# Kernel optimization log

Hardware: AMD Instinct MI355X
Metric: run time of the kernel (lower is better)

## Reference

```python
import jax, jax.numpy as jnp
import numpy as np

EPS = 1e-5

def inorm(x):
    # instance norm over time (last) axis; torch.std is unbiased (ddof=1)
    m = jnp.mean(x, axis=-1, keepdims=True)
    s = jnp.sqrt(jnp.var(x, axis=-1, ddof=1, keepdims=True))
    return (x - m) / (s + EPS)

def tinorm(x):
    # time-wise instance norm: normalize over channel axis (dim=1)
    m = jnp.mean(x, axis=1, keepdims=True)
    s = jnp.sqrt(jnp.var(x, axis=1, ddof=1, keepdims=True))
    return (x - m) / (s + EPS)

def adaptive_norm(src, trg, wq, wk, wv, norm_fn):
    # src, trg: [B,C,T]; wq/wk/wv: [out,in] as in nn.Linear
    temp = src.shape[1] ** 0.5
    q = jnp.einsum('bct,oc->bto', norm_fn(src), wq)        # [B,Ts,C]
    k = jnp.einsum('bct,oc->bto', norm_fn(trg), wk)        # [B,Tt,C]
    v = jnp.einsum('bct,oc->bto', trg, wv)                 # [B,Tt,C]
    attn = jax.nn.softmax(jnp.einsum('bsc,btc->bst', q / temp, k), axis=-1)
    mean = jnp.einsum('bst,btc->bsc', attn, v)             # attn-weighted mean
    var = jax.nn.relu(jnp.einsum('bst,btc->bsc', attn, v * v) - mean * mean)
    mean_c = jnp.mean(mean, axis=1)[:, :, None]            # [B,C,1]
    std_c = jnp.sqrt(jnp.mean(var, axis=1))[:, :, None]    # [B,C,1]
    return std_c * inorm(src) + mean_c

def sap(x, w, b):
    # self-attention pooling over axis 1; x: [B,N,C], w: [C], b: [1]
    a = jax.nn.softmax(jnp.einsum('bnc,c->bn', x, w) + b, axis=-1)
    return jnp.einsum('bnc,bn->bc', x, a)

def setup_inputs():
    key = jax.random.key(0)
    ks = jax.random.split(key, 24)
    B, C, Ts, Tt, S = 4, 512, 2048, 2048, 2048
    sc = 1.0 / np.sqrt(C).astype(np.float32)
    return {
        'src': jax.random.normal(ks[0], (B, C, Ts), jnp.float32),
        'trg': jax.random.normal(ks[1], (B, C, Tt), jnp.float32),
        'means': jax.random.normal(ks[2], (B, S, C), jnp.float32),
        'stds': jax.random.uniform(ks[3], (B, S, C), jnp.float32),
        'wq_t': jax.random.normal(ks[4], (C, C), jnp.float32) * sc,
        'wk_t': jax.random.normal(ks[5], (C, C), jnp.float32) * sc,
        'wv_t': jax.random.normal(ks[6], (C, C), jnp.float32) * sc,
        'wq_c': jax.random.normal(ks[7], (C, C), jnp.float32) * sc,
        'wk_c': jax.random.normal(ks[8], (C, C), jnp.float32) * sc,
        'wv_c': jax.random.normal(ks[9], (C, C), jnp.float32) * sc,
        'conv1_w': jax.random.normal(ks[10], (C, 2 * C), jnp.float32) * sc,
        'conv1_b': jax.random.normal(ks[11], (C,), jnp.float32) * 0.02,
        'conv2_w': jax.random.normal(ks[12], (C, C, 3), jnp.float32) * sc,
        'bn_g': jax.random.uniform(ks[13], (C,), jnp.float32, 0.5, 1.5),
        'bn_b': jax.random.normal(ks[14], (C,), jnp.float32) * 0.05,
        'bn_m': jax.random.normal(ks[15], (C,), jnp.float32) * 0.1,
        'bn_v': jax.random.uniform(ks[16], (C,), jnp.float32, 0.5, 1.5),
        'msap_w': jax.random.normal(ks[17], (C,), jnp.float32) * sc,
        'msap_b': jax.random.normal(ks[18], (1,), jnp.float32) * 0.02,
        'ssap_w': jax.random.normal(ks[19], (C,), jnp.float32) * sc,
        'ssap_b': jax.random.normal(ks[20], (1,), jnp.float32) * 0.02,
    }

def reference(src, trg, means, stds, wq_t, wk_t, wv_t, wq_c, wk_c, wv_c,
              conv1_w, conv1_b, conv2_w, bn_g, bn_b, bn_m, bn_v,
              msap_w, msap_b, ssap_w, ssap_b):
    src1 = adaptive_norm(src, trg, wq_t, wk_t, wv_t, tinorm)   # TAN
    src2 = adaptive_norm(src, trg, wq_c, wk_c, wv_c, inorm)    # CAN
    x = jnp.concatenate([src1, src2], axis=1)                  # [B,2C,T]
    # conv1: kernel_size=1 -> pointwise GEMM
    x = jnp.einsum('bct,oc->bot', x, conv1_w) + conv1_b[None, :, None]
    # conv2: Conv1d(k=3, pad=1, bias=False) + BatchNorm1d(eval) + ReLU
    x = jax.lax.conv_general_dilated(x, conv2_w, (1,), 'SAME',
                                     dimension_numbers=('NCH', 'OIH', 'NCH'))
    x = (x - bn_m[None, :, None]) * jax.lax.rsqrt(bn_v[None, :, None] + EPS)
    x = x * bn_g[None, :, None] + bn_b[None, :, None]
    x = jax.nn.relu(x)
    # GLAN
    mean = sap(means, msap_w, msap_b)[:, :, None]              # [B,C,1]
    std = sap(stds, ssap_w, ssap_b)[:, :, None]                # [B,C,1]
    return inorm(x) * std + mean
```

## Files before the change

kernel.cpp:

```cpp
#include <hip/hip_runtime.h>
#include <cstdint>
#include <cstddef>

#define B_ 4
#define C_ 512
#define T_ 2048
#define S_ 2048
#define EPSF 1e-5f

typedef __bf16 bf16;
typedef __attribute__((ext_vector_type(8))) __bf16 bf16x8;
typedef __attribute__((ext_vector_type(4))) float f32x4;

__device__ __forceinline__ bf16 f2b(float f){ return (bf16)f; }
__device__ __forceinline__ float b2f(bf16 h){ return (float)h; }

__device__ __forceinline__ void gl_lds16(const void* g, void* l){
  __builtin_amdgcn_global_load_lds((__attribute__((address_space(1))) void*)(g),
                                   (__attribute__((address_space(3))) void*)(l), 16, 0, 0);
}

__device__ __forceinline__ float wave_sum(float v){
#pragma unroll
  for (int o = 32; o; o >>= 1) v += __shfl_xor(v, o, 64);
  return v;
}
__device__ __forceinline__ float wave_max(float v){
#pragma unroll
  for (int o = 32; o; o >>= 1) v = fmaxf(v, __shfl_xor(v, o, 64));
  return v;
}

template<int EPI, int TNW, int GX = 0, int GY = 0, int NZ = 0>
__global__ void __launch_bounds__(256) gemm_nt(
    const bf16* __restrict__ A, const bf16* __restrict__ Bm, void* __restrict__ Cout,
    int K, int lda, int ldb, int ldc,
    long long sA, long long sB, long long sC, long long sCb,
    int zdivA, int zmodB, float scale,
    const float* __restrict__ rs, const float* __restrict__ rsh,
    const float* __restrict__ cbias,
    float* __restrict__ osum, float* __restrict__ osum2, long long sRs,
    float* __restrict__ ocol)
{
  constexpr int TN = TNW*32;
  __shared__ alignas(16) bf16 lA[128*64];
  __shared__ alignas(16) bf16 lB[TN*64];
  __shared__ float redcs[EPI == 3 ? 32*68 : 1];
  const int tid = threadIdx.x;

  int bxv, byv, z;
  if constexpr (GX > 0) {
    const int bid = blockIdx.x;
    const int xcd = bid & 7, slot = bid >> 3;
    constexpr int NB  = GX*GY;
    constexpr int ZPX = (NZ >= 8) ? NZ/8 : 1;
    constexpr int XPZ = (NZ >= 8) ? 1 : 8/NZ;
    z = (xcd / XPZ) * ZPX + ((ZPX > 1) ? slot / NB : 0);
    const int inner = (ZPX > 1) ? (slot % NB)
                                : (slot + (xcd % XPZ) * (NB / XPZ));
    bxv = inner % GX; byv = inner / GX;
  } else {
    bxv = blockIdx.x; byv = blockIdx.y; z = blockIdx.z;
  }

  const bf16* Ab = A + (long long)(z / zdivA) * sA;
  const bf16* Bb = Bm + (long long)(z % zmodB) * sB;
  const int m0 = byv*128, n0 = bxv*TN;
  const int lane = tid & 63, wvi = tid >> 6;
  const int wm = wvi >> 1, wn = wvi & 1;

  f32x4 acc[4][TNW] = {};

  const int lrow = tid >> 3;
  const int lcol = ((tid ^ lrow) & 7) * 8;
  const bf16* pa = Ab + (long long)(m0 + lrow)*lda + lcol;
  const bf16* pb = Bb + (long long)(n0 + lrow)*ldb + lcol;
  char* sa = (char*)lA + tid*16;
  char* sb = (char*)lB + tid*16;

  const int csg = tid >> 3, csph = tid & 7;
  float linv4[4];
  if (EPI == 3) {
#pragma unroll
    for (int rr = 0; rr < 4; ++rr)
      linv4[rr] = 1.f / rs[(long long)z*sRs + (m0 + csg*4 + rr)];
  }

  for (int k0 = 0; k0 < K; k0 += 64) {
#pragma unroll
    for (int it = 0; it < 4; ++it)
      gl_lds16(pa + (long long)it*32*lda + k0, sa + it*4096);
#pragma unroll
    for (int it = 0; it < TNW; ++it)
      gl_lds16(pb + (long long)it*32*ldb + k0, sb + it*4096);
    __syncthreads();
#pragma unroll
    for (int ks = 0; ks < 2; ++ks) {
      const int kq = ks*4 + (lane >> 4);
      bf16x8 af[4], bfr[TNW];
#pragma unroll
      for (int mt = 0; mt < 4; ++mt) {
        int r = wm*64 + mt*16 + (lane & 15);
        af[mt] = *(const bf16x8*)&lA[r*64 + ((kq ^ (r & 7))*8)];
      }
#pragma unroll
      for (int nt = 0; nt < TNW; ++nt) {
        int r = wn*(TNW*16) + nt*16 + (lane & 15);
        bfr[nt] = *(const bf16x8*)&lB[r*64 + ((kq ^ (r & 7))*8)];
      }
#pragma unroll
      for (int mt = 0; mt < 4; ++mt)
#pragma unroll
        for (int nt = 0; nt < TNW; ++nt)
          acc[mt][nt] = __builtin_amdgcn_mfma_f32_16x16x32_bf16(af[mt], bfr[nt], acc[mt][nt], 0, 0, 0);
    }
    bool own = false;
    if (EPI == 3) {
      own = ((k0 >> 6) & 3) == bxv;
      if (own) {
        float part[8] = {0.f,0.f,0.f,0.f,0.f,0.f,0.f,0.f};
#pragma unroll
        for (int rr = 0; rr < 4; ++rr) {
          const int r = csg*4 + rr;
          bf16x8 v = *(const bf16x8*)&lA[r*64 + ((csph ^ (r & 7))*8)];
          const float li = linv4[rr];
#pragma unroll
          for (int j = 0; j < 8; ++j) part[j] += b2f(v[j]) * li;
        }
#pragma unroll
        for (int j = 0; j < 8; ++j) redcs[csg*68 + csph*8 + j] = part[j];
      }
    }
    __syncthreads();
    if (EPI == 3) {
      if (own && tid < 64) {
        float s = 0.f;
#pragma unroll
        for (int g2 = 0; g2 < 32; ++g2) s += redcs[g2*68 + tid];
        atomicAdd(&ocol[(long long)z*lda + k0 + tid], s);
      }
    }
  }

  if (EPI == 3) {
    float* red2 = (float*)lA;
    const int cr = (lane >> 4)*4;
    float linv[4][4];
#pragma unroll
    for (int mt = 0; mt < 4; ++mt)
#pragma unroll
      for (int i = 0; i < 4; ++i)
        linv[mt][i] = 1.f / rs[(long long)z*sRs + (m0 + wm*64 + mt*16 + cr + i)];
    float s2[TNW];
#pragma unroll
    for (int nt = 0; nt < TNW; ++nt) {
      s2[nt] = 0.f;
#pragma unroll
      for (int mt = 0; mt < 4; ++mt)
#pragma unroll
        for (int i = 0; i < 4; ++i) {
          float v = acc[mt][nt][i] * linv[mt][i];
          s2[nt] += v*v;
        }
      s2[nt] += __shfl_xor(s2[nt], 16, 64);
      s2[nt] += __shfl_xor(s2[nt], 32, 64);
    }
    __syncthreads();
    if (lane < 16) {
#pragma unroll
      for (int nt = 0; nt < TNW; ++nt)
        red2[(wvi*TNW + nt)*16 + lane] = s2[nt];
    }
    __syncthreads();
    if (tid < TN) {
      const int wn2 = tid / (TNW*16), rem = tid % (TNW*16);
      float v = red2[wn2*(TNW*16) + rem] + red2[(2+wn2)*(TNW*16) + rem];
      atomicAdd(&osum2[sCb*z + n0 + tid], v);
    }
    return;
  }

  const int cr = (lane >> 4)*4, cc = lane & 15;
#pragma unroll
  for (int mt = 0; mt < 4; ++mt) {
#pragma unroll
    for (int i = 0; i < 4; ++i) {
      const int mm = m0 + wm*64 + mt*16 + cr + i;
      float rsum = 0.f, rsum2 = 0.f;
#pragma unroll
      for (int nt = 0; nt < TNW; ++nt) {
        const int nn = n0 + wn*(TNW*16) + nt*16 + cc;
        float v = acc[mt][nt][i];
        const long long co = sC*z + (long long)mm*ldc + nn;
        if (EPI == 0) {
          v *= scale;
          if (cbias) v += cbias[sCb*z + nn];
          ((bf16*)Cout)[co] = f2b(v);
        } else if (EPI == 2) {
          v = fmaxf(v*rs[mm] + rsh[mm], 0.f);
          ((float*)Cout)[co] = v;
          rsum += v; rsum2 += v*v;
        } else if (EPI == 4) {
          v = __expf(v);
          ((bf16*)Cout)[co] = f2b(v);
          rsum += v;
        } else if (EPI == 5) {
          v = v*rs[(long long)z*sRs + mm] + rsh[(long long)z*sRs + mm]*cbias[sCb*z + nn];
          ((bf16*)Cout)[co] = f2b(v);
        }
      }
      if (EPI == 2 || EPI == 4) {
        rsum += __shfl_xor(rsum, 1, 64); rsum += __shfl_xor(rsum, 2, 64);
        rsum += __shfl_xor(rsum, 4, 64); rsum += __shfl_xor(rsum, 8, 64);
        if (EPI == 2) {
          rsum2 += __shfl_xor(rsum2, 1, 64); rsum2 += __shfl_xor(rsum2, 2, 64);
          rsum2 += __shfl_xor(rsum2, 4, 64); rsum2 += __shfl_xor(rsum2, 8, 64);
        }
        if (cc == 0) {
          atomicAdd(&osum[(long long)z*sRs + mm], rsum);
          if (EPI == 2) atomicAdd(&osum2[(long long)z*sRs + mm], rsum2);
        }
      }
    }
  }
}

__global__ void __launch_bounds__(512, 2) qk_exp_k(
    const bf16* __restrict__ QK, bf16* __restrict__ P, float* __restrict__ lsum)
{
  __shared__ alignas(16) char lds[65536];
  const int tid = threadIdx.x;
  const int bid = blockIdx.x;
  const int xcd = bid & 7, slot = bid >> 3;
  const int z  = (xcd >> 1) + ((slot >> 5) << 2);
  const int t  = (slot & 31) + ((xcd & 1) << 5);
  const int by = t >> 3, bx = t & 7;
  const int ph = z >> 2, b = z & 3;
  const bf16* Qb = QK + (long long)(b*2 + ph) * (2048LL*512);
  const bf16* Kb = QK + (long long)(8 + b*2 + ph) * (2048LL*512);
  const int m0 = by * 256, n0 = bx * 256;
  const int lane = tid & 63, wvi = tid >> 6;
  const int wm = wvi >> 2, wn = wvi & 3;
  const int l15 = lane & 15, lq = lane >> 4;
  const int swz = l15 & 7;

  f32x4 acc[8][4] = {};

  const int lr = tid >> 3;
  const int lc = ((tid ^ lr) & 7) * 8;
  const bf16* pa = Qb + (long long)(m0 + lr)*512 + lc;
  const bf16* pb = Kb + (long long)(n0 + lr)*512 + lc;

  for (int kt = 0; kt < 8; ++kt) {
    {
      char* da = (char*)lds + tid*16;
      const bf16* ga = pa + kt*64;
      const bf16* gb = pb + kt*64;
#pragma unroll
      for (int it = 0; it < 4; ++it) gl_lds16(ga + it*64*512, da + it*8192);
#pragma unroll
      for (int it = 0; it < 4; ++it) gl_lds16(gb + it*64*512, da + 32768 + it*8192);
    }
    asm volatile("s_waitcnt vmcnt(0)" ::: "memory");
    __builtin_amdgcn_s_barrier();

    const bf16* lA = (const bf16*)lds;
    const bf16* lB = lA + 16384;

    bf16x8 af[4], bfr[4];
#pragma unroll
    for (int half = 0; half < 4; ++half) {
      const int ks = half >> 1, mg = (half & 1) * 4;
      const int kq = ks*4 + lq;
      const int ko = (kq ^ swz) * 8;
      if ((half & 1) == 0) {
#pragma unroll
        for (int nt = 0; nt < 4; ++nt)
          bfr[nt] = *(const bf16x8*)&lB[(wn*64 + nt*16 + l15)*64 + ko];
      }
#pragma unroll
      for (int mt = 0; mt < 4; ++mt)
        af[mt] = *(const bf16x8*)&lA[(wm*128 + (mg + mt)*16 + l15)*64 + ko];
      __builtin_amdgcn_s_barrier();
      __builtin_amdgcn_s_setprio(1);
#pragma unroll
      for (int mt = 0; mt < 4; ++mt)
#pragma unroll
        for (int nt = 0; nt < 4; ++nt)
          acc[mg + mt][nt] = __builtin_amdgcn_mfma_f32_16x16x32_bf16(
              af[mt], bfr[nt], acc[mg + mt][nt], 0, 0, 0);
      __builtin_amdgcn_s_setprio(0);
      __builtin_amdgcn_s_barrier();
    }
  }

  const long long zT = (long long)z * 2048;
  bf16* Cb = P + zT * 2048;
  float* lrw = lsum + zT;
  const int cr = lq * 4;
#pragma unroll
  for (int mt = 0; mt < 8; ++mt) {
#pragma unroll
    for (int i = 0; i < 4; ++i) {
      const int mm = m0 + wm*128 + mt*16 + cr + i;
      float rsum = 0.f;
#pragma unroll
      for (int nt = 0; nt < 4; ++nt) {
        const int nn = n0 + wn*64 + nt*16 + l15;
        float v = __expf(acc[mt][nt][i]);
        Cb[(long long)mm*2048 + nn] = f2b(v);
        rsum += v;
      }
      rsum += __shfl_xor(rsum, 1, 64); rsum += __shfl_xor(rsum, 2, 64);
      rsum += __shfl_xor(rsum, 4, 64); rsum += __shfl_xor(rsum, 8, 64);
      if (l15 == 0) atomicAdd(&lrw[mm], rsum);
    }
  }
}

__global__ void __launch_bounds__(256) transform_stats_k(
    const float* __restrict__ src, const float* __restrict__ trg,
    bf16* __restrict__ XT, float* __restrict__ rsum, float* __restrict__ rsum2,
    float* __restrict__ csum, float* __restrict__ csum2)
{
  __shared__ float tile[64][33];
  __shared__ float rp1[64][4], rp2[64][4];
  __shared__ float cp1[32][8], cp2[32][8];
  const int z = blockIdx.z, t0 = blockIdx.x*32, c0 = blockIdx.y*64;
  const int is_t = z >= B_, b = z & (B_-1);
  const float* X = is_t ? trg : src;
  const int tid = threadIdx.x;
  const int tx = tid & 31, cy = tid >> 5;
#pragma unroll
  for (int it = 0; it < 8; ++it) {
    const int cl = cy + it*8;
    tile[cl][tx] = X[((long long)b*C_ + c0 + cl)*T_ + t0 + tx];
  }
  __syncthreads();
  const int l32 = tid & 31, tq = tid >> 5;
#pragma unroll
  for (int r = 0; r < 4; ++r) {
    const int tl = r*8 + tq;
    bf16 b0 = f2b(tile[2*l32][tl]), b1 = f2b(tile[2*l32+1][tl]);
    unsigned short u0, u1;
    __builtin_memcpy(&u0, &b0, 2); __builtin_memcpy(&u1, &b1, 2);
    const unsigned int pk = (unsigned int)u0 | ((unsigned int)u1 << 16);
    *(unsigned int*)&XT[((long long)z*T_ + t0 + tl)*C_ + c0 + 2*l32] = pk;
  }
  {
    const int cl = tid >> 2, g = tid & 3;
    float s1 = 0.f, s2 = 0.f;
#pragma unroll
    for (int k = 0; k < 8; ++k){ float v = tile[cl][g + 4*k]; s1 += v; s2 += v*v; }
    rp1[cl][g] = s1; rp2[cl][g] = s2;
  }
  {
    const int tl = tid >> 3, g = tid & 7;
    float s1 = 0.f, s2 = 0.f;
#pragma unroll
    for (int k = 0; k < 8; ++k){ float v = tile[g + 8*k][tl]; s1 += v; s2 += v*v; }
    cp1[tl][g] = s1; cp2[tl][g] = s2;
  }
  __syncthreads();
  if (tid < 64) {
    float s1 = rp1[tid][0]+rp1[tid][1]+rp1[tid][2]+rp1[tid][3];
    float s2 = rp2[tid][0]+rp2[tid][1]+rp2[tid][2]+rp2[tid][3];
    atomicAdd(&rsum[z*C_ + c0 + tid], s1);
    atomicAdd(&rsum2[z*C_ + c0 + tid], s2);
  } else if (tid < 96) {
    const int tl = tid - 64;
    float s1 = 0.f, s2 = 0.f;
#pragma unroll
    for (int g = 0; g < 8; ++g){ s1 += cp1[tl][g]; s2 += cp2[tl][g]; }
    atomicAdd(&csum[z*T_ + t0 + tl], s1);
    atomicAdd(&csum2[z*T_ + t0 + tl], s2);
  }
}

__global__ void __launch_bounds__(256) statfin_k(
    const float* __restrict__ rsum, const float* __restrict__ rsum2,
    const float* __restrict__ csum, const float* __restrict__ csum2,
    float* __restrict__ inm, float* __restrict__ ins,
    float* __restrict__ tnm, float* __restrict__ tns)
{
  const int i = blockIdx.x*256 + threadIdx.x;
  if (i < 2*B_*C_) {
    const float s1 = rsum[i], s2 = rsum2[i];
    const float m = s1 * (1.f/T_);
    const float var = (s2 - s1*m) * (1.f/(T_-1));
    inm[i] = m; ins[i] = sqrtf(fmaxf(var, 0.f));
  } else {
    const int j = i - 2*B_*C_;
    const float s1 = csum[j], s2 = csum2[j];
    const float m = s1 * (1.f/C_);
    const float var = (s2 - s1*m) * (1.f/(C_-1));
    tnm[j] = m; tns[j] = sqrtf(fmaxf(var, 0.f));
  }
}

__global__ void __launch_bounds__(256) foldqk_k(
    const float* __restrict__ wq_c, const float* __restrict__ wq_t,
    const float* __restrict__ wk_c, const float* __restrict__ wk_t,
    const float* __restrict__ inm, const float* __restrict__ ins,
    bf16* __restrict__ W, float* __restrict__ cb)
{
  __shared__ float r1[4];
  const int o = blockIdx.x, z = blockIdx.y;
  const int side = z >> 3, b = (z >> 1) & 3, ph = z & 1;
  const float* w = side ? (ph ? wk_t : wk_c) : (ph ? wq_t : wq_c);
  const float sc = side ? 1.f : 0.044194173824159216f;
  const int ofs = (side*B_ + b)*C_;
  float acc = 0.f;
  for (int c = threadIdx.x; c < C_; c += 256) {
    float wv = w[o*C_ + c] * sc;
    float out, contrib;
    if (ph == 0) {
      float ri = 1.f / (ins[ofs + c] + EPSF);
      out = wv * ri;
      contrib = -out * inm[ofs + c];
    } else {
      out = wv;
      contrib = wv;
    }
    W[((long long)z*C_ + o)*C_ + c] = f2b(out);
    acc += contrib;
  }
  acc = wave_sum(acc);
  const int lane = threadIdx.x & 63, wq = threadIdx.x >> 6;
  if (!lane) r1[wq] = acc;
  __syncthreads();
  if (threadIdx.x == 0) cb[z*C_ + o] = r1[0]+r1[1]+r1[2]+r1[3];
}

__global__ void __launch_bounds__(256) rsfill_k(
    const float* __restrict__ tnm, const float* __restrict__ tns,
    float* __restrict__ rsq, float* __restrict__ rshq)
{
  const int z = blockIdx.y, t = blockIdx.x*256 + threadIdx.x;
  const int side = z >> 3, b = (z >> 1) & 3, ph = z & 1;
  float rv, rh;
  if (ph == 0) { rv = 1.f; rh = 1.f; }
  else {
    const int ofs = (side*B_ + b)*T_;
    float r = 1.f / (tns[ofs + t] + EPSF);
    rv = r; rh = -tnm[ofs + t] * r;
  }
  rsq[z*T_ + t] = rv; rshq[z*T_ + t] = rh;
}

__global__ void __launch_bounds__(256) softmax_row_k(const float* __restrict__ X, float* __restrict__ O)
{
  __shared__ float red[4];
  const long long row = blockIdx.x;
  const float* x = X + row*T_ + threadIdx.x*8;
  float v[8];
  f32x4 a0 = *(const f32x4*)x;
  f32x4 a1 = *(const f32x4*)(x + 4);
#pragma unroll
  for (int j = 0; j < 4; ++j){ v[j] = a0[j]; v[4+j] = a1[j]; }
  float m = -3.4e38f;
#pragma unroll
  for (int j = 0; j < 8; ++j) m = fmaxf(m, v[j]);
  m = wave_max(m);
  const int lane = threadIdx.x & 63, w = threadIdx.x >> 6;
  if (!lane) red[w] = m;
  __syncthreads();
  m = fmaxf(fmaxf(red[0], red[1]), fmaxf(red[2], red[3]));
  __syncthreads();
  float s = 0.f;
#pragma unroll
  for (int j = 0; j < 8; ++j){ v[j] = __expf(v[j] - m); s += v[j]; }
  s = wave_sum(s);
  if (!lane) red[w] = s;
  __syncthreads();
  s = red[0]+red[1]+red[2]+red[3];
  const float inv = 1.f/s;
  float* o = O + row*T_ + threadIdx.x*8;
#pragma unroll
  for (int j = 0; j < 8; ++j) o[j] = v[j]*inv;
}

__global__ void __launch_bounds__(256) vv_fin_k(const float* __restrict__ cs,
    const bf16* __restrict__ VT,
    const float* __restrict__ m2sum, float* __restrict__ meanc, float* __restrict__ stdc)
{
  __shared__ float r1[4], r2[4];
  const int c = blockIdx.x, z = blockIdx.y;
  const bf16* vr = VT + ((long long)z*C_ + c)*T_;
  const float* w = cs + z*T_;
  float a1 = 0.f, a2 = 0.f;
  for (int t = threadIdx.x; t < T_; t += 256){
    float v = b2f(vr[t]); float wt = w[t];
    a1 += wt*v; a2 += wt*v*v;
  }
  a1 = wave_sum(a1); a2 = wave_sum(a2);
  const int lane = threadIdx.x & 63, wq = threadIdx.x >> 6;
  if (!lane){ r1[wq] = a1; r2[wq] = a2; }
  __syncthreads();
  if (threadIdx.x == 0){
    a1 = r1[0]+r1[1]+r1[2]+r1[3];
    a2 = r2[0]+r2[1]+r2[2]+r2[3];
    const int idx = z*C_ + c;
    meanc[idx] = a1 * (1.f/S_);
    float var = (a2 - m2sum[idx]) * (1.f/S_);
    stdc[idx] = sqrtf(fmaxf(var, 0.f));
  }
}

__global__ void __launch_bounds__(256) weff_k(const float* __restrict__ w1,
    const float* __restrict__ b1, const float* __restrict__ sdt, const float* __restrict__ sdc,
    const float* __restrict__ mct, const float* __restrict__ mcc,
    const float* __restrict__ inm, const float* __restrict__ ins,
    bf16* __restrict__ Weff, float* __restrict__ beff)
{
  __shared__ float r1[4];
  const int o = blockIdx.x, b = blockIdx.y;
  const int ofs = b*C_;
  float accb = 0.f;
  for (int c = threadIdx.x; c < C_; c += 256) {
    float wa = w1[o*2*C_ + c], wb = w1[o*2*C_ + C_ + c];
    float s = wa*sdt[b*C_+c] + wb*sdc[b*C_+c];
    float w2 = s / (ins[ofs + c] + EPSF);
    Weff[((long long)(b*C_ + o))*C_ + c] = f2b(w2);
    accb += wa*mct[b*C_+c] + wb*mcc[b*C_+c] - w2*inm[ofs + c];
  }
  accb = wave_sum(accb);
  const int lane = threadIdx.x & 63, w = threadIdx.x >> 6;
  if (!lane) r1[w] = accb;
  __syncthreads();
  if (threadIdx.x == 0) beff[b*C_ + o] = b1[o] + r1[0]+r1[1]+r1[2]+r1[3];
}

__global__ void __launch_bounds__(256) w2r_k(const float* __restrict__ w2,
    const float* __restrict__ g, const float* __restrict__ be,
    const float* __restrict__ mu, const float* __restrict__ va,
    bf16* __restrict__ W2r, float* __restrict__ bnsc, float* __restrict__ bnsh)
{
  const int o = blockIdx.x;
  for (int c = threadIdx.x; c < C_; c += 256)
#pragma unroll
    for (int dt = 0; dt < 3; ++dt)
      W2r[(long long)o*3*C_ + dt*C_ + c] = f2b(w2[((long long)o*C_ + c)*3 + dt]);
  if (threadIdx.x == 0) {
    float s = g[o] * rsqrtf(va[o] + EPSF);
    bnsc[o] = s;
    bnsh[o] = be[o] - mu[o]*s;
  }
}

__global__ void __launch_bounds__(256) castv_k(const float* __restrict__ a0,
    const float* __restrict__ a1, bf16* __restrict__ o)
{
  const int i = blockIdx.x*256 + threadIdx.x;
  o[i] = f2b(((i >> 18) ? a1 : a0)[i & 262143]);
}

__global__ void __launch_bounds__(256) zero_pad_k(bf16* __restrict__ x1p)
{
  const int i = blockIdx.x*256 + threadIdx.x;
  const int b = i >> 10, rem = i & 1023;
  const long long row = (rem >> 9) ? (T_+1) : 0;
  const int c = rem & (C_-1);
  x1p[((long long)b*(T_+2) + row)*C_ + c] = f2b(0.f);
}

__global__ void __launch_bounds__(256) zero_f32_k(float* __restrict__ p)
{
  p[blockIdx.x*256 + threadIdx.x] = 0.f;
}

__global__ void __launch_bounds__(256) sap_logit_k(const float* __restrict__ means,
    const float* __restrict__ stds, const float* __restrict__ mw, const float* __restrict__ sw,
    const float* __restrict__ mb, const float* __restrict__ sb, float* __restrict__ out)
{
  const int n = blockIdx.x*4 + (threadIdx.x >> 6);
  const int z = blockIdx.y;
  const int sel = z >= B_, b = z & (B_-1);
  const float* x = sel ? stds : means;
  const float* w = sel ? sw : mw;
  const int lane = threadIdx.x & 63;
  const float* p = x + ((long long)b*S_ + n)*C_;
  float a = 0.f;
  for (int c = lane; c < C_; c += 64) a += p[c]*w[c];
  a = wave_sum(a);
  if (!lane) out[z*S_ + n] = a + (sel ? sb[0] : mb[0]);
}

__global__ void __launch_bounds__(256) sap_wsum_k(const float* __restrict__ means,
    const float* __restrict__ stds, const float* __restrict__ a, float* __restrict__ out)
{
  const int c = blockIdx.x*256 + threadIdx.x;
  const int z = blockIdx.z;
  const int sel = z >= B_, b = z & (B_-1);
  const float* x = sel ? stds : means;
  const long long n0 = (long long)blockIdx.y*256;
  const float* p = x + ((long long)b*S_ + n0)*C_ + c;
  const float* aw = a + z*S_ + n0;
  float acc = 0.f;
  for (int n = 0; n < 256; ++n) acc += p[(long long)n*C_] * aw[n];
  atomicAdd(&out[z*C_ + c], acc);
}

__global__ void __launch_bounds__(256) final_k(const float* __restrict__ y,
    const float* __restrict__ ysum, const float* __restrict__ y2sum,
    const float* __restrict__ sapms, float* __restrict__ out)
{
  const long long i = (long long)(blockIdx.x*256 + threadIdx.x) * 4;
  const long long r = i >> 11;
  const float s1 = ysum[r], s2 = y2sum[r];
  const float m = s1 * (1.f/T_);
  const float var = (s2 - s1*m) * (1.f/(T_-1));
  const float inv = 1.f/(sqrtf(fmaxf(var, 0.f)) + EPSF);
  const float mn = sapms[r], sd = sapms[B_*C_ + r];
  const f32x4 v = *(const f32x4*)(y + i);
  f32x4 o;
#pragma unroll
  for (int j = 0; j < 4; ++j) o[j] = (v[j] - m)*inv*sd + mn;
  *(f32x4*)(out + i) = o;
}

extern "C" void kernel_launch(void* const* d_in, const int* in_sizes, int n_in,
                              void* d_out, int out_size, void* d_ws, size_t ws_size,
                              hipStream_t stream)
{
  (void)in_sizes; (void)n_in; (void)out_size; (void)ws_size;
  const float* src    = (const float*)d_in[0];
  const float* trg    = (const float*)d_in[1];
  const float* means  = (const float*)d_in[2];
  const float* stds   = (const float*)d_in[3];
  const float* conv1w = (const float*)d_in[10];
  const float* conv1b = (const float*)d_in[11];
  const float* conv2w = (const float*)d_in[12];
  const float* bn_g   = (const float*)d_in[13];
  const float* bn_b   = (const float*)d_in[14];
  const float* bn_m   = (const float*)d_in[15];
  const float* bn_v   = (const float*)d_in[16];
  const float* msap_w = (const float*)d_in[17];
  const float* msap_b = (const float*)d_in[18];
  const float* ssap_w = (const float*)d_in[19];
  const float* ssap_b = (const float*)d_in[20];

  const long long BTC = (long long)B_*T_*C_;
  const long long TC  = (long long)T_*C_;

  char* p = (char*)d_ws;
  auto take = [&](size_t n)->char*{ char* r = p; p += (n + 255) & ~(size_t)255; return r; };

  bf16* P2  = (bf16*)take((size_t)2*B_*S_*T_*2);
  bf16* QK4 = (bf16*)take((size_t)16*TC*2);
  bf16* VT2 = (bf16*)take((size_t)2*BTC*2);
  bf16* WQeff = (bf16*)take((size_t)16*C_*C_*2);
  bf16* WVb = (bf16*)take((size_t)2*C_*C_*2);
  bf16* Weff= (bf16*)take((size_t)B_*C_*C_*2);
  bf16* W2r = (bf16*)take((size_t)C_*3*C_*2);
  bf16* x1p = (bf16*)take((size_t)B_*(T_+2)*C_*2);
  float* y  = (float*)take((size_t)B_*C_*T_*4);
  bf16* XT  = (bf16*)y;
  float* colsum = (float*)take(2*B_*T_*4);
  float* msum   = (float*)take(2*B_*C_*4);
  float* m2sum  = (float*)take(2*B_*C_*4);
  float* sapms  = (float*)take(2*B_*C_*4);
  float* lrow   = (float*)take(2*B_*S_*4);
  float* ysum   = (float*)take(B_*C_*4);
  float* y2sum  = (float*)take(B_*C_*4);
  float* rsum   = (float*)take(2*B_*C_*4);
  float* rsum2  = (float*)take(2*B_*C_*4);
  float* csum   = (float*)take(2*B_*T_*4);
  float* csum2  = (float*)take(2*B_*T_*4);
  float* tnm = (float*)take(2*B_*T_*4);
  float* tns = (float*)take(2*B_*T_*4);
  float* inm = (float*)take(2*B_*C_*4);
  float* ins = (float*)take(2*B_*C_*4);
  float* meanc = (float*)take(2*B_*C_*4);
  float* stdc  = (float*)take(2*B_*C_*4);
  float* beff  = (float*)take(B_*C_*4);
  float* bnsc  = (float*)take(C_*4);
  float* bnsh  = (float*)take(C_*4);
  float* sapl  = (float*)take(2*B_*S_*4);
  float* sapa  = (float*)take(2*B_*S_*4);
  float* cbq   = (float*)take(16*C_*4);
  float* rsq   = (float*)take(16*T_*4);
  float* rshq  = (float*)take(16*T_*4);
  (void)msum;

  dim3 blk(256);

  zero_f32_k<<<352, blk, 0, stream>>>(colsum);
  castv_k<<<2048, blk, 0, stream>>>((const float*)d_in[9], (const float*)d_in[6], WVb);
  w2r_k<<<C_, blk, 0, stream>>>(conv2w, bn_g, bn_b, bn_m, bn_v, W2r, bnsc, bnsh);
  transform_stats_k<<<dim3(T_/32, C_/64, 2*B_), blk, 0, stream>>>(src, trg, XT,
      rsum, rsum2, csum, csum2);
  statfin_k<<<80, blk, 0, stream>>>(rsum, rsum2, csum, csum2, inm, ins, tnm, tns);
  foldqk_k<<<dim3(C_, 16), blk, 0, stream>>>((const float*)d_in[7], (const float*)d_in[4],
      (const float*)d_in[8], (const float*)d_in[5], inm, ins, WQeff, cbq);
  rsfill_k<<<dim3(T_/256, 16), blk, 0, stream>>>(tnm, tns, rsq, rshq);
  zero_pad_k<<<16, blk, 0, stream>>>(x1p);

  gemm_nt<5,4,4,16,16><<<dim3(1024), blk, 0, stream>>>(XT, WQeff, QK4,
      C_, C_, C_, C_, TC, (long long)C_*C_, TC, C_,
      2, 16, 1.f, rsq, rshq, cbq, nullptr, nullptr, T_, nullptr);
  gemm_nt<0,2,32,4,8><<<dim3(1024), blk, 0, stream>>>(WVb, XT + 4*TC, VT2,
      C_, C_, C_, T_, (long long)C_*C_, TC, (long long)C_*T_, 0, 4, 4, 1.f,
      nullptr, nullptr, nullptr, nullptr, nullptr, 0, nullptr);
  qk_exp_k<<<dim3(512), dim3(512), 0, stream>>>(QK4, P2, lrow);
  gemm_nt<3,4,4,16,8><<<dim3(512), blk, 0, stream>>>(P2, VT2, nullptr,
      T_, T_, T_, 0, (long long)S_*T_, (long long)C_*T_, 0, C_, 1, 8, 1.f,
      lrow, nullptr, nullptr, nullptr, m2sum, S_, colsum);
  vv_fin_k<<<dim3(C_, 2*B_), blk, 0, stream>>>(colsum, VT2, m2sum, meanc, stdc);

  weff_k<<<dim3(C_, B_), blk, 0, stream>>>(conv1w, conv1b,
      stdc + B_*C_, stdc, meanc + B_*C_, meanc, inm, ins, Weff, beff);
  gemm_nt<0,2,8,16,4><<<dim3(512), blk, 0, stream>>>(XT, Weff, x1p + C_,
      C_, C_, C_, C_, TC, (long long)C_*C_, (long long)(T_+2)*C_, C_,
      1, 8, 1.f, nullptr, nullptr, beff, nullptr, nullptr, 0, nullptr);
  gemm_nt<2,2,32,4,4><<<dim3(512), blk, 0, stream>>>(W2r, x1p, y,
      3*C_, 3*C_, C_, T_, 0, (long long)(T_+2)*C_, (long long)C_*T_, 0,
      1, 8, 1.f, bnsc, bnsh, nullptr, ysum, y2sum, C_, nullptr);

  sap_logit_k<<<dim3(S_/4, 2*B_), blk, 0, stream>>>(means, stds, msap_w, ssap_w,
      msap_b, ssap_b, sapl);
  softmax_row_k<<<2*B_, blk, 0, stream>>>(sapl, sapa);
  sap_wsum_k<<<dim3(C_/256, S_/256, 2*B_), blk, 0, stream>>>(means, stds, sapa, sapms);

  final_k<<<4096, blk, 0, stream>>>(y, ysum, y2sum, sapms, (float*)d_out);
}
```

Before: 413.1 us.

## Double-buffer QK LDS loads and stage exp output through LDS for coalesced stores

The QK-exp GEMM kernel now double-buffers its LDS tiles, issuing the next k-step's global-to-LDS loads before waiting on the current ones, so memory latency overlaps the MFMA work. The epilogue also writes the exp'd bf16 tile into LDS first and then stores 16-byte rows to global memory, replacing scattered 2-byte stores. The LDS footprint grows to about 132 KB per block, which, with launch_bounds(512,2), likely limits residency to a single block per CU and reduces occupancy.

```diff
diff --git a/kernel.cpp b/kernel.cpp
--- a/kernel.cpp
+++ b/kernel.cpp
@@ -228,7 +228,7 @@
 __global__ void __launch_bounds__(512, 2) qk_exp_k(
     const bf16* __restrict__ QK, bf16* __restrict__ P, float* __restrict__ lsum)
 {
-  __shared__ alignas(16) char lds[65536];
+  __shared__ alignas(16) char lds[135168];
   const int tid = threadIdx.x;
   const int bid = blockIdx.x;
   const int xcd = bid & 7, slot = bid >> 3;
@@ -251,20 +251,28 @@
   const bf16* pa = Qb + (long long)(m0 + lr)*512 + lc;
   const bf16* pb = Kb + (long long)(n0 + lr)*512 + lc;
 
+  auto STAGE = [&](int bb, int kt) {
+    char* da = (char*)lds + bb*65536 + tid*16;
+    const bf16* ga = pa + kt*64;
+    const bf16* gb = pb + kt*64;
+#pragma unroll
+    for (int it = 0; it < 4; ++it) gl_lds16(ga + it*64*512, da + it*8192);
+#pragma unroll
+    for (int it = 0; it < 4; ++it) gl_lds16(gb + it*64*512, da + 32768 + it*8192);
+  };
+
+  STAGE(0, 0);
   for (int kt = 0; kt < 8; ++kt) {
-    {
-      char* da = (char*)lds + tid*16;
-      const bf16* ga = pa + kt*64;
-      const bf16* gb = pb + kt*64;
-#pragma unroll
-      for (int it = 0; it < 4; ++it) gl_lds16(ga + it*64*512, da + it*8192);
-#pragma unroll
-      for (int it = 0; it < 4; ++it) gl_lds16(gb + it*64*512, da + 32768 + it*8192);
-    }
-    asm volatile("s_waitcnt vmcnt(0)" ::: "memory");
+    const int cur = kt & 1;
+    if (kt < 7) {
+      STAGE(cur ^ 1, kt + 1);
+      asm volatile("s_waitcnt vmcnt(8)" ::: "memory");
+    } else {
+      asm volatile("s_waitcnt vmcnt(0)" ::: "memory");
+    }
     __builtin_amdgcn_s_barrier();
 
-    const bf16* lA = (const bf16*)lds;
+    const bf16* lA = (const bf16*)(lds + cur*65536);
     const bf16* lB = lA + 16384;
 
     bf16x8 af[4], bfr[4];
@@ -294,27 +302,37 @@
     }
   }
 
+  constexpr int LDC = 264;
+  bf16* lC = (bf16*)lds;
   const long long zT = (long long)z * 2048;
-  bf16* Cb = P + zT * 2048;
   float* lrw = lsum + zT;
   const int cr = lq * 4;
 #pragma unroll
   for (int mt = 0; mt < 8; ++mt) {
 #pragma unroll
     for (int i = 0; i < 4; ++i) {
-      const int mm = m0 + wm*128 + mt*16 + cr + i;
+      const int mmL = wm*128 + mt*16 + cr + i;
       float rsum = 0.f;
 #pragma unroll
       for (int nt = 0; nt < 4; ++nt) {
-        const int nn = n0 + wn*64 + nt*16 + l15;
+        const int nnL = wn*64 + nt*16 + l15;
         float v = __expf(acc[mt][nt][i]);
-        Cb[(long long)mm*2048 + nn] = f2b(v);
+        lC[mmL*LDC + nnL] = f2b(v);
         rsum += v;
       }
       rsum += __shfl_xor(rsum, 1, 64); rsum += __shfl_xor(rsum, 2, 64);
       rsum += __shfl_xor(rsum, 4, 64); rsum += __shfl_xor(rsum, 8, 64);
-      if (l15 == 0) atomicAdd(&lrw[mm], rsum);
-    }
+      if (l15 == 0) atomicAdd(&lrw[m0 + mmL], rsum);
+    }
+  }
+  __syncthreads();
+  bf16* Cb = P + zT * 2048;
+#pragma unroll
+  for (int j = 0; j < 16; ++j) {
+    const int flat = j*512 + tid;
+    const int r = flat >> 5, c16 = flat & 31;
+    const f32x4 v = *(const f32x4*)&lC[r*LDC + c16*8];
+    *(f32x4*)&Cb[(long long)(m0 + r)*2048 + n0 + c16*8] = v;
   }
 }
 
```

Result: faster. 397.7 us, median of 2 (-3.7%).
